# Kernel tuning notes

Measured on AMD Instinct MI355X. Metric: run time of the kernel, lower is better.

## Reference

```python
import jax, jax.numpy as jnp
import numpy as np

EPS = 1e-7  # SimplifiedLayerNorm eps


def setup_inputs() -> dict:
    key = jax.random.key(0)
    k1, k2 = jax.random.split(key)
    x = jax.random.normal(k1, (8, 2048, 64), dtype=jnp.float32)   # [B, T, d]
    W = jax.random.normal(k2, (2048, 8), dtype=jnp.float32)       # [T, H] per-distance, per-head Toeplitz weights
    return {"x": x, "W": W}


def _l2norm(v):
    return v / (jnp.linalg.norm(v, axis=-1, keepdims=True) + EPS)


def reference(x, W):
    B, T, d = x.shape
    H = W.shape[1]
    # pad one zero token: [B, T+1, d]
    xp = jnp.concatenate([x, jnp.zeros((B, 1, d), x.dtype)], axis=1)
    idx = jnp.arange(T + 1)
    dist = idx[:, None] - idx[None, :]                 # [T+1, T+1], row - col
    # Toeplitz logits: W[dist, h] for 0 <= dist < T; the single dist==T entry
    # (bottom-left corner) is left at its initial 0.0; dist < 0 is causally masked.
    Wd = W[jnp.clip(dist, 0, T - 1)]                   # [T+1, T+1, H]
    dist3 = dist[..., None]
    logits = jnp.where(dist3 < 0, -jnp.inf,
                       jnp.where(dist3 >= T, jnp.zeros((), x.dtype), Wd))
    probs = jax.nn.softmax(logits, axis=1)             # softmax over columns (dim=-1 of W_h)
    v = jnp.einsum('tsh,bsd->hbtd', probs, xp)         # [H, B, T+1, d]
    v = _l2norm(v)
    V = jnp.concatenate([v, xp[None]], axis=0)         # [H+1, B, T+1, d]
    V = _l2norm(V)
    return V
```

## Files before the change

kernel.cpp:

```cpp
#include <hip/hip_runtime.h>

#define EPS 1e-7f
#define T_DIM 2048
#define TP1   2049
#define H_DIM 8
#define B_DIM 8

#define NFRAG 146
#define NST   33
#define AREG  10240
#define BUFSZ 18432
#define RSTRIDE 66

#define J1_BLOCKS 292
#define J2_BLOCKS 264
#define J3_BLOCKS 4098
#define MM_BLOCKS 1088

typedef short v8s __attribute__((ext_vector_type(8)));
typedef float v4f __attribute__((ext_vector_type(4)));

static __device__ __forceinline__ unsigned short f2bf(float f) {
  union { float f; unsigned u; } v; v.f = f;
  unsigned r = v.u + 0x7fffu + ((v.u >> 16) & 1u);
  return (unsigned short)(r >> 16);
}

static __device__ __forceinline__ void load_lds16(const void* g, void* l) {
  __builtin_amdgcn_global_load_lds(
      (const __attribute__((address_space(1))) unsigned int*)g,
      (__attribute__((address_space(3))) unsigned int*)l, 16, 0, 0);
}

__global__ __launch_bounds__(256) void prep(const float* __restrict__ x,
                                            const float* __restrict__ W,
                                            unsigned short* __restrict__ fragA,
                                            unsigned short* __restrict__ xT,
                                            float* __restrict__ out) {
  __shared__ float tile[64][65];
  int bid = blockIdx.x;
  if (bid < J1_BLOCKS) {
    int tid = bid * 256 + threadIdx.x;
    int blk = tid >> 6, lane = tid & 63;
    int h = blk / NFRAG, fbp = blk - h * NFRAG;
    int b0 = fbp * 16 - 160;
    int lm = lane & 15, quad = lane >> 4;
    v8s frag;
    #pragma unroll
    for (int j = 0; j < 8; ++j) {
      int d = b0 + lm - 8 * quad - j;
      float v = 0.0f;
      if (d >= 0 && d < T_DIM) v = __expf(W[d * H_DIM + h]);
      else if (d == T_DIM) v = 1.0f;
      frag[j] = (short)f2bf(v);
    }
    *(v8s*)(fragA + (size_t)tid * 8) = frag;
    return;
  }
  bid -= J1_BLOCKS;
  if (bid < J2_BLOCKS) {
    int b = bid / NST, st = bid - b * NST;
    int s0 = st * 64;
    int tid = threadIdx.x;
    int c = tid & 63, r4 = tid >> 6;
    #pragma unroll
    for (int i = 0; i < 16; ++i) {
      int sl = r4 * 16 + i;
      int s = s0 + sl;
      tile[sl][c] = (s < T_DIM) ? x[((size_t)b * T_DIM + s) * 64 + c] : 0.0f;
    }
    __syncthreads();
    int dd = tid >> 2, pb = (tid & 3) * 2;
    unsigned short* dst = xT + ((size_t)(b * NST + st) << 12) + dd * 64;
    #pragma unroll
    for (int e = 0; e < 2; ++e) {
      int p = pb + e;
      int sb = ((p ^ (dd & 7)) << 3);
      v8s o;
      #pragma unroll
      for (int j = 0; j < 8; ++j) o[j] = (short)f2bf(tile[sb + j][dd]);
      *(v8s*)(dst + p * 8) = o;
    }
    return;
  }
  bid -= J2_BLOCKS;
  {
    int row = bid * 4 + (threadIdx.x >> 6);
    if (row >= B_DIM * TP1) return;
    int b = row / TP1, t = row - b * TP1;
    int dd = threadIdx.x & 63;
    float v = (t < T_DIM) ? x[((size_t)b * T_DIM + t) * 64 + dd] : 0.0f;
    float ss = v * v;
    ss += __shfl_xor(ss, 1);  ss += __shfl_xor(ss, 2);
    ss += __shfl_xor(ss, 4);  ss += __shfl_xor(ss, 8);
    ss += __shfl_xor(ss, 16); ss += __shfl_xor(ss, 32);
    float inv = 1.0f / (sqrtf(ss) + EPS);
    __builtin_nontemporal_store(v * inv,
        &out[(((size_t)(H_DIM * B_DIM + b) * TP1 + t) << 6) + dd]);
  }
}

__global__ __launch_bounds__(256, 4) void toeplitz_mm(const unsigned short* __restrict__ fragA,
                                                      const unsigned short* __restrict__ xT,
                                                      float* __restrict__ out) {
  __shared__ __align__(16) char smem[2][BUFSZ];

  const int lane = threadIdx.x & 63;
  const int w    = threadIdx.x >> 6;
  const int wm   = w & 1;
  const int wk   = w >> 1;
  const int lm   = lane & 15;
  const int quad = lane >> 4;

  const int bid = blockIdx.x;
  const int h   = bid & 7;
  const int b   = (bid >> 3) & 7;
  const int k   = bid >> 6;
  const int lvl = (k < 4) ? 2 * k : (k < 12) ? 23 - 2 * k : (k < 16) ? 2 * k - 16 : 16;
  const int t0  = T_DIM - lvl * 128;
  const int tw  = t0 + 64 * wm;
  const bool active = (tw <= T_DIM);
  const int cap = min(tw + 32, T_DIM);

  const int NS = (min(t0 + 96, T_DIM) >> 6) + 1;

  const unsigned short* fA = fragA + (size_t)h * NFRAG * 512 + lane * 8;

#define STAGE(bufi, it) do {                                                   \
    int _s0 = (it) << 6;                                                       \
    int _E0p = ((t0 - _s0 + 32) >> 4) + 6;                                     \
    const unsigned short* _A = fA + (size_t)_E0p * 512;                        \
    const unsigned short* _B = xT + ((size_t)(b * NST + (_s0 >> 6)) << 12) + lane * 8; \
    char* _lb = &smem[bufi][0];                                                \
    _Pragma("unroll")                                                          \
    for (int _i = 0; _i < 5; ++_i) {                                           \
      int _u = w + _i * 4;                                                     \
      if (_u < 18) {                                                           \
        const unsigned short* _src = (_u < 10)                                 \
            ? (_A + (size_t)_u * 512)                                          \
            : (_B + ((_u - 10) * 512));                                        \
        load_lds16(_src, _lb + _u * 1024);                                     \
      }                                                                        \
    }                                                                          \
  } while (0)

  v4f acc[4][4] = {};

  STAGE(0, 0);
  STAGE(1, 1);
  int buf = 0;
  for (int it = 0; it < NS; ++it) {
    if (it < NS - 1) {
      if (w < 2) asm volatile("s_waitcnt vmcnt(5)" ::: "memory");
      else       asm volatile("s_waitcnt vmcnt(4)" ::: "memory");
    } else {
      asm volatile("s_waitcnt vmcnt(0)" ::: "memory");
    }
    __builtin_amdgcn_s_barrier();
    __builtin_amdgcn_sched_barrier(0);

    const char* Ab = &smem[buf][0];
    const char* Bb = Ab + AREG;
    int c0 = (it << 6) + 32 * wk;
    __builtin_amdgcn_s_setprio(1);
    if (active && c0 <= cap) {
      v8s af[4], bf[4];
      #pragma unroll
      for (int mt = 0; mt < 4; ++mt)
        af[mt] = *(const v8s*)(Ab + (2 + 4 * wm - 2 * wk + mt) * 1024 + lane * 16);
      #pragma unroll
      for (int nt = 0; nt < 4; ++nt)
        bf[nt] = *(const v8s*)(Bb + nt * 2048 + lm * 128 +
                               ((((wk << 2) | quad) ^ (lm & 7)) << 4));
      #pragma unroll
      for (int mt = 0; mt < 4; ++mt)
        #pragma unroll
        for (int nt = 0; nt < 4; ++nt)
          acc[mt][nt] = __builtin_amdgcn_mfma_f32_16x16x32_bf16(af[mt], bf[nt],
                                                                acc[mt][nt], 0, 0, 0);
    }
    __builtin_amdgcn_s_setprio(0);
    __builtin_amdgcn_sched_barrier(0);
    __builtin_amdgcn_s_barrier();
    if (it + 2 < NS) STAGE(buf, it + 2);
    buf ^= 1;
  }

  float* red0 = (float*)&smem[0][0];
  float* bufp = red0 + wm * (64 * RSTRIDE);
  if (wk == 1) {
    #pragma unroll
    for (int mt = 0; mt < 4; ++mt)
      #pragma unroll
      for (int r = 0; r < 4; ++r) {
        int row = 16 * mt + 4 * quad + r;
        #pragma unroll
        for (int nt = 0; nt < 4; ++nt)
          bufp[row * RSTRIDE + 16 * nt + lm] = acc[mt][nt][r];
      }
  }
  __syncthreads();
  if (wk != 0) return;

  #pragma unroll
  for (int mt = 0; mt < 4; ++mt) {
    #pragma unroll
    for (int r = 0; r < 4; ++r) {
      int row = 16 * mt + 4 * quad + r;
      #pragma unroll
      for (int nt = 0; nt < 4; ++nt)
        acc[mt][nt][r] += bufp[row * RSTRIDE + 16 * nt + lm];
    }
  }

  #pragma unroll
  for (int mt = 0; mt < 4; ++mt) {
    #pragma unroll
    for (int r = 0; r < 4; ++r) {
      float ss = 0.0f;
      #pragma unroll
      for (int nt = 0; nt < 4; ++nt) { float a = acc[mt][nt][r]; ss += a * a; }
      ss += __shfl_xor(ss, 1);
      ss += __shfl_xor(ss, 2);
      ss += __shfl_xor(ss, 4);
      ss += __shfl_xor(ss, 8);
      int t = tw + 16 * mt + 4 * quad + r;
      if (t <= T_DIM) {
        float n1 = sqrtf(ss);
        float u  = n1 / (n1 + EPS);
        float inv = 1.0f / ((n1 + EPS) * (u + EPS));
        float* op = out + (((size_t)(h * B_DIM + b) * TP1 + t) << 6) + lm;
        #pragma unroll
        for (int nt = 0; nt < 4; ++nt)
          __builtin_nontemporal_store(acc[mt][nt][r] * inv, op + 16 * nt);
      }
    }
  }
#undef STAGE
}

extern "C" void kernel_launch(void* const* d_in, const int* in_sizes, int n_in,
                              void* d_out, int out_size, void* d_ws, size_t ws_size,
                              hipStream_t stream) {
  const float* x = (const float*)d_in[0];
  const float* W = (const float*)d_in[1];
  float* out = (float*)d_out;

  unsigned short* xT    = (unsigned short*)d_ws;
  unsigned short* fragA = (unsigned short*)((char*)d_ws + 2162688);

  hipLaunchKernelGGL(prep, dim3(J1_BLOCKS + J2_BLOCKS + J3_BLOCKS), dim3(256), 0, stream,
                     x, W, fragA, xT, out);
  hipLaunchKernelGGL(toeplitz_mm, dim3(MM_BLOCKS), dim3(256), 0, stream,
                     fragA, xT, out);
}
```

Baseline: 103.6 us.

## Widen Toeplitz MMA blocks to two batches and 128-wide K stages

Each matmul block now runs 8 waves over two batches and steps 128 columns of K per stage instead of 64. The Toeplitz A fragments loaded to LDS are shared across both batches and both K halves, which halves the grid and the number of barrier-synchronised stages. In exchange the LDS per block grows to about 92KB, so fewer blocks fit per CU, and the padding of the fragment and xT buffers in the prep kernel changes to match.

New measurement: 110.8 us. 1.07x slower.

```diff
diff --git a/kernel.cpp b/kernel.cpp
--- a/kernel.cpp
+++ b/kernel.cpp
@@ -6,16 +6,16 @@
 #define H_DIM 8
 #define B_DIM 8
 
-#define NFRAG 146
-#define NST   33
-#define AREG  10240
-#define BUFSZ 18432
+#define NFRAG 148
+#define NST   34
+#define AREG  14336
+#define BUFSZ 47104
 #define RSTRIDE 66
 
-#define J1_BLOCKS 292
-#define J2_BLOCKS 264
+#define J1_BLOCKS 296
+#define J2_BLOCKS 272
 #define J3_BLOCKS 4098
-#define MM_BLOCKS 1088
+#define MM_BLOCKS 544
 
 typedef short v8s __attribute__((ext_vector_type(8)));
 typedef float v4f __attribute__((ext_vector_type(4)));
@@ -43,7 +43,7 @@
     int tid = bid * 256 + threadIdx.x;
     int blk = tid >> 6, lane = tid & 63;
     int h = blk / NFRAG, fbp = blk - h * NFRAG;
-    int b0 = fbp * 16 - 160;
+    int b0 = fbp * 16 - 192;
     int lm = lane & 15, quad = lane >> 4;
     v8s frag;
     #pragma unroll
@@ -100,45 +100,53 @@
   }
 }
 
-__global__ __launch_bounds__(256, 4) void toeplitz_mm(const unsigned short* __restrict__ fragA,
-                                                      const unsigned short* __restrict__ xT,
-                                                      float* __restrict__ out) {
+__global__ __launch_bounds__(512) void toeplitz_mm(const unsigned short* __restrict__ fragA,
+                                                   const unsigned short* __restrict__ xT,
+                                                   float* __restrict__ out) {
   __shared__ __align__(16) char smem[2][BUFSZ];
 
   const int lane = threadIdx.x & 63;
   const int w    = threadIdx.x >> 6;
   const int wm   = w & 1;
-  const int wk   = w >> 1;
+  const int wb   = (w >> 1) & 1;
+  const int wk   = w >> 2;
   const int lm   = lane & 15;
   const int quad = lane >> 4;
 
   const int bid = blockIdx.x;
   const int h   = bid & 7;
-  const int b   = (bid >> 3) & 7;
-  const int k   = bid >> 6;
-  const int lvl = (k < 4) ? 2 * k : (k < 12) ? 23 - 2 * k : (k < 16) ? 2 * k - 16 : 16;
+  const int bg  = (bid >> 3) & 3;
+  const int k   = bid >> 5;
+  const int lvl = (k < 8) ? k : ((k < 16) ? 23 - k : 16);
   const int t0  = T_DIM - lvl * 128;
   const int tw  = t0 + 64 * wm;
+  const int b   = bg * 2 + wb;
   const bool active = (tw <= T_DIM);
   const int cap = min(tw + 32, T_DIM);
 
-  const int NS = (min(t0 + 96, T_DIM) >> 6) + 1;
+  const int NS = (min(t0 + 96, T_DIM) >> 7) + 1;
 
   const unsigned short* fA = fragA + (size_t)h * NFRAG * 512 + lane * 8;
 
 #define STAGE(bufi, it) do {                                                   \
-    int _s0 = (it) << 6;                                                       \
-    int _E0p = ((t0 - _s0 + 32) >> 4) + 6;                                     \
-    const unsigned short* _A = fA + (size_t)_E0p * 512;                        \
-    const unsigned short* _B = xT + ((size_t)(b * NST + (_s0 >> 6)) << 12) + lane * 8; \
+    int _S = (it) << 7;                                                        \
+    int _Pb = ((t0 - _S + 32) >> 4) + 4;                                       \
+    const unsigned short* _A = fA + (size_t)_Pb * 512;                         \
+    int _st0 = _S >> 6;                                                        \
     char* _lb = &smem[bufi][0];                                                \
     _Pragma("unroll")                                                          \
-    for (int _i = 0; _i < 5; ++_i) {                                           \
-      int _u = w + _i * 4;                                                     \
-      if (_u < 18) {                                                           \
-        const unsigned short* _src = (_u < 10)                                 \
-            ? (_A + (size_t)_u * 512)                                          \
-            : (_B + ((_u - 10) * 512));                                        \
+    for (int _i = 0; _i < 6; ++_i) {                                           \
+      int _u = w + _i * 8;                                                     \
+      if (_u < 46) {                                                           \
+        const unsigned short* _src;                                            \
+        if (_u < 14) {                                                         \
+          _src = _A + (size_t)_u * 512;                                        \
+        } else {                                                               \
+          int _v = _u - 14;                                                    \
+          int _bsel = _v >> 4, _stsel = (_v >> 3) & 1, _p = _v & 7;            \
+          _src = xT + ((size_t)((bg * 2 + _bsel) * NST + _st0 + _stsel) << 12) \
+                 + _p * 512 + lane * 8;                                        \
+        }                                                                      \
         load_lds16(_src, _lb + _u * 1024);                                     \
       }                                                                        \
     }                                                                          \
@@ -147,12 +155,12 @@
   v4f acc[4][4] = {};
 
   STAGE(0, 0);
-  STAGE(1, 1);
+  if (NS > 1) STAGE(1, 1);
   int buf = 0;
   for (int it = 0; it < NS; ++it) {
     if (it < NS - 1) {
-      if (w < 2) asm volatile("s_waitcnt vmcnt(5)" ::: "memory");
-      else       asm volatile("s_waitcnt vmcnt(4)" ::: "memory");
+      if (w < 6) asm volatile("s_waitcnt vmcnt(6)" ::: "memory");
+      else       asm volatile("s_waitcnt vmcnt(5)" ::: "memory");
     } else {
       asm volatile("s_waitcnt vmcnt(0)" ::: "memory");
     }
@@ -160,24 +168,29 @@
     __builtin_amdgcn_sched_barrier(0);
 
     const char* Ab = &smem[buf][0];
-    const char* Bb = Ab + AREG;
-    int c0 = (it << 6) + 32 * wk;
+    const char* Bb = Ab + AREG + (wb * 2 + wk) * 8192;
+    int S = it << 7;
     __builtin_amdgcn_s_setprio(1);
-    if (active && c0 <= cap) {
-      v8s af[4], bf[4];
-      #pragma unroll
-      for (int mt = 0; mt < 4; ++mt)
-        af[mt] = *(const v8s*)(Ab + (2 + 4 * wm - 2 * wk + mt) * 1024 + lane * 16);
-      #pragma unroll
-      for (int nt = 0; nt < 4; ++nt)
-        bf[nt] = *(const v8s*)(Bb + nt * 2048 + lm * 128 +
-                               ((((wk << 2) | quad) ^ (lm & 7)) << 4));
-      #pragma unroll
-      for (int mt = 0; mt < 4; ++mt)
+    v8s af6[6];
+    #pragma unroll
+    for (int e = 0; e < 6; ++e)
+      af6[e] = *(const v8s*)(Ab + (4 + 4 * wm - 4 * wk + e) * 1024 + lane * 16);
+    #pragma unroll
+    for (int kkl = 0; kkl < 2; ++kkl) {
+      int c = S + 64 * wk + 32 * kkl;
+      if (active && c <= cap) {
+        v8s bf[4];
         #pragma unroll
         for (int nt = 0; nt < 4; ++nt)
-          acc[mt][nt] = __builtin_amdgcn_mfma_f32_16x16x32_bf16(af[mt], bf[nt],
-                                                                acc[mt][nt], 0, 0, 0);
+          bf[nt] = *(const v8s*)(Bb + nt * 2048 + lm * 128 +
+                                 ((((kkl << 2) | quad) ^ (lm & 7)) << 4));
+        #pragma unroll
+        for (int mt = 0; mt < 4; ++mt)
+          #pragma unroll
+          for (int nt = 0; nt < 4; ++nt)
+            acc[mt][nt] = __builtin_amdgcn_mfma_f32_16x16x32_bf16(
+                af6[(kkl ? 0 : 2) + mt], bf[nt], acc[mt][nt], 0, 0, 0);
+      }
     }
     __builtin_amdgcn_s_setprio(0);
     __builtin_amdgcn_sched_barrier(0);
@@ -186,8 +199,7 @@
     buf ^= 1;
   }
 
-  float* red0 = (float*)&smem[0][0];
-  float* bufp = red0 + wm * (64 * RSTRIDE);
+  float* red = (float*)&smem[0][0] + (wm * 2 + wb) * (64 * RSTRIDE);
   if (wk == 1) {
     #pragma unroll
     for (int mt = 0; mt < 4; ++mt)
@@ -196,7 +208,7 @@
         int row = 16 * mt + 4 * quad + r;
         #pragma unroll
         for (int nt = 0; nt < 4; ++nt)
-          bufp[row * RSTRIDE + 16 * nt + lm] = acc[mt][nt][r];
+          red[row * RSTRIDE + 16 * nt + lm] = acc[mt][nt][r];
       }
   }
   __syncthreads();
@@ -209,9 +221,11 @@
       int row = 16 * mt + 4 * quad + r;
       #pragma unroll
       for (int nt = 0; nt < 4; ++nt)
-        acc[mt][nt][r] += bufp[row * RSTRIDE + 16 * nt + lm];
-    }
-  }
+        acc[mt][nt][r] += red[row * RSTRIDE + 16 * nt + lm];
+    }
+  }
+
+  if (!active) return;
 
   #pragma unroll
   for (int mt = 0; mt < 4; ++mt) {
@@ -247,10 +261,10 @@
   float* out = (float*)d_out;
 
   unsigned short* xT    = (unsigned short*)d_ws;
-  unsigned short* fragA = (unsigned short*)((char*)d_ws + 2162688);
+  unsigned short* fragA = (unsigned short*)((char*)d_ws + 2228224);
 
   hipLaunchKernelGGL(prep, dim3(J1_BLOCKS + J2_BLOCKS + J3_BLOCKS), dim3(256), 0, stream,
                      x, W, fragA, xT, out);
-  hipLaunchKernelGGL(toeplitz_mm, dim3(MM_BLOCKS), dim3(256), 0, stream,
+  hipLaunchKernelGGL(toeplitz_mm, dim3(MM_BLOCKS), dim3(512), 0, stream,
                      fragA, xT, out);
 }
```

## Load MFMA fragments directly from global into registers, dropping LDS staging

Applied to the files above, without the earlier changes.

Replaces the LDS double-buffered global_load_lds pipeline and its per-iteration barriers with per-wave direct global-to-register fragment loads, double-buffered in registers. Each wave now runs its own K loop with no block-wide synchronisation and keeps LDS only for the final split-K reduction. The aim is to remove barrier stalls and LDS traffic. The cost is redundant global/L2 reads, since waves no longer share staged A/B tiles, and more VGPR pressure under the 4-blocks-per-SM launch bound.

Result: slower. 159.4 us (+53.9%).

```diff
diff --git a/kernel.cpp b/kernel.cpp
--- a/kernel.cpp
+++ b/kernel.cpp
@@ -8,8 +8,6 @@
 
 #define NFRAG 146
 #define NST   33
-#define AREG  10240
-#define BUFSZ 18432
 #define RSTRIDE 66
 
 #define J1_BLOCKS 292
@@ -24,12 +22,6 @@
   union { float f; unsigned u; } v; v.f = f;
   unsigned r = v.u + 0x7fffu + ((v.u >> 16) & 1u);
   return (unsigned short)(r >> 16);
-}
-
-static __device__ __forceinline__ void load_lds16(const void* g, void* l) {
-  __builtin_amdgcn_global_load_lds(
-      (const __attribute__((address_space(1))) unsigned int*)g,
-      (__attribute__((address_space(3))) unsigned int*)l, 16, 0, 0);
 }
 
 __global__ __launch_bounds__(256) void prep(const float* __restrict__ x,
@@ -103,7 +95,7 @@
 __global__ __launch_bounds__(256, 4) void toeplitz_mm(const unsigned short* __restrict__ fragA,
                                                       const unsigned short* __restrict__ xT,
                                                       float* __restrict__ out) {
-  __shared__ __align__(16) char smem[2][BUFSZ];
+  __shared__ float red[2][64 * RSTRIDE];
 
   const int lane = threadIdx.x & 63;
   const int w    = threadIdx.x >> 6;
@@ -122,72 +114,50 @@
   const bool active = (tw <= T_DIM);
   const int cap = min(tw + 32, T_DIM);
 
-  const int NS = (min(t0 + 96, T_DIM) >> 6) + 1;
-
-  const unsigned short* fA = fragA + (size_t)h * NFRAG * 512 + lane * 8;
-
-#define STAGE(bufi, it) do {                                                   \
-    int _s0 = (it) << 6;                                                       \
-    int _E0p = ((t0 - _s0 + 32) >> 4) + 6;                                     \
-    const unsigned short* _A = fA + (size_t)_E0p * 512;                        \
-    const unsigned short* _B = xT + ((size_t)(b * NST + (_s0 >> 6)) << 12) + lane * 8; \
-    char* _lb = &smem[bufi][0];                                                \
+  const unsigned short* fA = fragA + ((size_t)h * NFRAG) * 512 + lane * 8;
+  const int swz = lm * 128 + ((((wk << 2) | quad) ^ (lm & 7)) << 4);
+
+#define LOAD_A(dst, c0v) do {                                                  \
+    const unsigned short* _p = fA + (size_t)((tw - (c0v) + 160) >> 4) * 512;   \
+    dst[0] = *(const v8s*)(_p);                                                \
+    dst[1] = *(const v8s*)(_p + 512);                                          \
+    dst[2] = *(const v8s*)(_p + 1024);                                         \
+    dst[3] = *(const v8s*)(_p + 1536); } while (0)
+#define LOAD_B(dst, c0v) do {                                                  \
+    const char* _cb = (const char*)(xT + ((size_t)(b * NST + ((c0v) >> 6)) << 12)) + swz; \
+    dst[0] = *(const v8s*)(_cb);                                               \
+    dst[1] = *(const v8s*)(_cb + 2048);                                        \
+    dst[2] = *(const v8s*)(_cb + 4096);                                        \
+    dst[3] = *(const v8s*)(_cb + 6144); } while (0)
+#define DO_MFMA(fa, fb) do {                                                   \
     _Pragma("unroll")                                                          \
-    for (int _i = 0; _i < 5; ++_i) {                                           \
-      int _u = w + _i * 4;                                                     \
-      if (_u < 18) {                                                           \
-        const unsigned short* _src = (_u < 10)                                 \
-            ? (_A + (size_t)_u * 512)                                          \
-            : (_B + ((_u - 10) * 512));                                        \
-        load_lds16(_src, _lb + _u * 1024);                                     \
-      }                                                                        \
-    }                                                                          \
-  } while (0)
+    for (int mt = 0; mt < 4; ++mt)                                             \
+      _Pragma("unroll")                                                        \
+      for (int nt = 0; nt < 4; ++nt)                                           \
+        acc[mt][nt] = __builtin_amdgcn_mfma_f32_16x16x32_bf16(fa[mt], fb[nt],  \
+                                                              acc[mt][nt], 0, 0, 0); } while (0)
 
   v4f acc[4][4] = {};
 
-  STAGE(0, 0);
-  STAGE(1, 1);
-  int buf = 0;
-  for (int it = 0; it < NS; ++it) {
-    if (it < NS - 1) {
-      if (w < 2) asm volatile("s_waitcnt vmcnt(5)" ::: "memory");
-      else       asm volatile("s_waitcnt vmcnt(4)" ::: "memory");
-    } else {
-      asm volatile("s_waitcnt vmcnt(0)" ::: "memory");
-    }
-    __builtin_amdgcn_s_barrier();
-    __builtin_amdgcn_sched_barrier(0);
-
-    const char* Ab = &smem[buf][0];
-    const char* Bb = Ab + AREG;
-    int c0 = (it << 6) + 32 * wk;
-    __builtin_amdgcn_s_setprio(1);
-    if (active && c0 <= cap) {
-      v8s af[4], bf[4];
-      #pragma unroll
-      for (int mt = 0; mt < 4; ++mt)
-        af[mt] = *(const v8s*)(Ab + (2 + 4 * wm - 2 * wk + mt) * 1024 + lane * 16);
-      #pragma unroll
-      for (int nt = 0; nt < 4; ++nt)
-        bf[nt] = *(const v8s*)(Bb + nt * 2048 + lm * 128 +
-                               ((((wk << 2) | quad) ^ (lm & 7)) << 4));
-      #pragma unroll
-      for (int mt = 0; mt < 4; ++mt)
-        #pragma unroll
-        for (int nt = 0; nt < 4; ++nt)
-          acc[mt][nt] = __builtin_amdgcn_mfma_f32_16x16x32_bf16(af[mt], bf[nt],
-                                                                acc[mt][nt], 0, 0, 0);
-    }
-    __builtin_amdgcn_s_setprio(0);
-    __builtin_amdgcn_sched_barrier(0);
-    __builtin_amdgcn_s_barrier();
-    if (it + 2 < NS) STAGE(buf, it + 2);
-    buf ^= 1;
-  }
-
-  float* red0 = (float*)&smem[0][0];
-  float* bufp = red0 + wm * (64 * RSTRIDE);
+  if (active) {
+    v8s a0[4], a1[4], b0[4], b1[4];
+    int c0 = 32 * wk;
+    LOAD_A(a0, c0); LOAD_B(b0, c0);
+    for (;;) {
+      bool more = (c0 + 64 <= cap);
+      if (more) { LOAD_A(a1, c0 + 64); LOAD_B(b1, c0 + 64); }
+      DO_MFMA(a0, b0);
+      if (!more) break;
+      c0 += 64;
+      bool more2 = (c0 + 64 <= cap);
+      if (more2) { LOAD_A(a0, c0 + 64); LOAD_B(b0, c0 + 64); }
+      DO_MFMA(a1, b1);
+      if (!more2) break;
+      c0 += 64;
+    }
+  }
+
+  float* bufp = red[wm];
   if (wk == 1) {
     #pragma unroll
     for (int mt = 0; mt < 4; ++mt)
@@ -212,6 +182,8 @@
         acc[mt][nt][r] += bufp[row * RSTRIDE + 16 * nt + lm];
     }
   }
+
+  if (!active) return;
 
   #pragma unroll
   for (int mt = 0; mt < 4; ++mt) {
@@ -236,7 +208,9 @@
       }
     }
   }
-#undef STAGE
+#undef LOAD_A
+#undef LOAD_B
+#undef DO_MFMA
 }
 
 extern "C" void kernel_launch(void* const* d_in, const int* in_sizes, int n_in,
```
